# Kernel tuning notes

Measured on AMD Instinct MI355X. Metric: run time of the kernel, lower is better.

Reference implementation:

```python
import jax, jax.numpy as jnp
import numpy as np

STATE_DIM = 64   # state_dim (N), N/2 complex modes
KLEN = 128       # L, learned impulse-response length
CH = 1           # channel_dim
BATCH = 32
T = 1048576      # sequence length (T > L -> FFT branch)
DT_MIN, DT_MAX = 0.001, 0.1


def setup_inputs() -> dict:
    key = jax.random.key(0)
    ks = jax.random.split(key, 7)
    N2 = STATE_DIM // 2
    x = jax.random.normal(ks[0], (BATCH, CH, T), dtype=jnp.float32)
    # HiPPO initialization: w = -0.5 + i * (1/pi) * N * (N/(1+2k) - 1)
    k = np.arange(N2)
    w_real = np.broadcast_to(np.float32(-0.5), (CH, N2)).copy()
    w_imag = np.broadcast_to(
        ((1.0 / np.pi) * STATE_DIM * (STATE_DIM / (1.0 + 2.0 * k) - 1.0)).astype(np.float32),
        (CH, N2)).copy()
    log_dt = (jax.random.uniform(ks[1], (CH, 1), dtype=jnp.float32)
              * (np.log(DT_MAX) - np.log(DT_MIN)) + np.log(DT_MIN))
    C_real = jax.random.normal(ks[2], (CH, 1, N2), dtype=jnp.float32) * 0.1
    C_imag = jax.random.normal(ks[3], (CH, 1, N2), dtype=jnp.float32) * 0.1
    B_real = jax.random.normal(ks[4], (CH, N2), dtype=jnp.float32)
    B_imag = jax.random.normal(ks[5], (CH, N2), dtype=jnp.float32)
    nrm = jnp.sqrt(jnp.sum(B_real ** 2 + B_imag ** 2, axis=-1, keepdims=True))
    B_real, B_imag = B_real / nrm, B_imag / nrm
    D = jax.random.normal(ks[6], (CH,), dtype=jnp.float32) * 0.1
    return {"azimuth_data": x,
            "w_real": jnp.asarray(w_real), "w_imag": jnp.asarray(w_imag),
            "log_dt": log_dt,
            "C_real": C_real, "C_imag": C_imag,
            "B_real": B_real, "B_imag": B_imag,
            "D": D}


def _ssm_kernel(w_real, w_imag, log_dt, C_real, C_imag, B_real, B_imag, D, L):
    """Vectorized equivalent of the per-step power recurrence: h_k = Re(sum_n C_n B_n A_n^k)."""
    w = w_real + 1j * w_imag                      # (CH, N2) complex eigenvalues
    dt = jnp.exp(log_dt)                          # (CH, 1)
    Cc = C_real + 1j * C_imag                     # (CH, 1, N2)
    Bc = B_real + 1j * B_imag                     # (CH, N2)
    dtA = dt[..., None] * w                       # (CH,1,1)*(CH,N2) -> (CH,1,N2)
    # coefficients C.squeeze(1) * B, with the same broadcast as torch: (CH,N2)*(CH,1,N2)->(CH,1,N2)
    coef = jnp.squeeze(Cc, axis=1) * (jnp.ones_like(dtA) * Bc)   # (CH,1,N2)
    ks = jnp.arange(L, dtype=dtA.real.dtype)                      # (L,)
    Ak = jnp.exp(dtA[..., None] * ks)                             # (CH,1,N2,L) = A_discrete**k
    h = jnp.real(jnp.sum(coef[..., None] * Ak, axis=-2))          # (CH,1,L)
    h = h.at[..., 0].add(D)                                       # hk[0] += D (broadcast (CH,1)+(CH,))
    return h[:, None]                                             # unsqueeze(1) -> (CH,1,1,L)


def reference(azimuth_data, w_real, w_imag, log_dt, C_real, C_imag, B_real, B_imag, D):
    Bsz, Cn, Tn = azimuth_data.shape
    kernel = _ssm_kernel(w_real, w_imag, log_dt, C_real, C_imag, B_real, B_imag, D, KLEN)
    pad = KLEN - 1
    x_padded = jnp.pad(azimuth_data, ((0, 0), (0, 0), (pad, 0)))   # causal left-pad
    L_conv = x_padded.shape[-1]
    x_f = jnp.fft.rfft(x_padded, n=L_conv)                         # (B, CH, F)
    k_f = jnp.fft.rfft(kernel, n=L_conv)                           # (CH, 1, 1, F)
    y_f = x_f * k_f                                                # broadcast -> (CH, B, 1, F)
    focused = jnp.fft.irfft(y_f, n=L_conv)[..., :Tn]               # (CH, B, 1, T) — matches torch broadcast
    return focused
```

## Files before the change

### kernel.cpp

```cpp
#include <hip/hip_runtime.h>

#define T_LEN  1048576
#define NROWS  32
#define NTAPS  128
#define N2     32
#define BLOCK  256
#define SEG    4096
#define SEGS_PER_ROW 256
#define HALO   256
#define NCH    11
#define STG_F32 (SEG + HALO)
#define STG_Q4  (STG_F32 / 4)
#define EPI_F32 (32 * 36)

typedef __attribute__((ext_vector_type(8)))  _Float16 half8;
typedef __attribute__((ext_vector_type(2)))  __fp16   fp16x2;
typedef __attribute__((ext_vector_type(16))) float    f32x16;

__device__ __forceinline__ int swz16(int q) { return q ^ ((q >> 3) & 7); }

__global__ __launch_bounds__(NTAPS) void ssm_taps(
    const float* __restrict__ w_real, const float* __restrict__ w_imag,
    const float* __restrict__ log_dt,
    const float* __restrict__ C_real, const float* __restrict__ C_imag,
    const float* __restrict__ B_real, const float* __restrict__ B_imag,
    const float* __restrict__ Dp, float* __restrict__ ws) {
  __shared__ float hsh[NTAPS];
  const int k = threadIdx.x;
  const float dt = expf(log_dt[0]);
  const float kf = (float)k;
  float acc = 0.f;
  for (int n = 0; n < N2; ++n) {
    const float a  = dt * w_real[n];
    const float b  = dt * w_imag[n];
    const float cr = C_real[n], ci = C_imag[n];
    const float br = B_real[n], bi = B_imag[n];
    const float coef_r = cr * br - ci * bi;
    const float coef_i = cr * bi + ci * br;
    const float e = expf(a * kf);
    float s, c;
    sincosf(b * kf, &s, &c);
    acc += e * (coef_r * c - coef_i * s);
  }
  if (k == 0) acc += Dp[0];
  ws[k]  = acc;
  hsh[k] = acc;
  __syncthreads();
  if (k < 64) {
    _Float16* AH = (_Float16*)(ws + NTAPS);
    const int m = k & 31, g = k >> 5;
    for (int c = 0; c < NCH; ++c)
      for (int i = 0; i < 8; ++i) {
        const int idx = m + 129 - 16 * c - 8 * g - i;
        const float v = (idx >= 0 && idx < NTAPS) ? hsh[idx] : 0.f;
        AH[(c * 64 + k) * 8 + i] = (_Float16)v;
      }
  }
}

__global__ __launch_bounds__(BLOCK, 5) void ssm_conv(
    const float* __restrict__ x, const float* __restrict__ ws,
    float* __restrict__ out) {
  __shared__ __align__(16) unsigned char smem[4 * EPI_F32 * 4];

  const int tid  = threadIdx.x;
  const int lane = tid & 63;
  const int wid  = tid >> 6;
  const int p    = lane & 31, g = lane >> 5;
  const int row  = blockIdx.x >> 8;
  const int jb   = blockIdx.x & 255;
  const int n0   = jb * SEG;
  const float* __restrict__ xrow = x + (size_t)row * T_LEN;

  half8 A[NCH];
  const half8* __restrict__ wsA = (const half8*)(ws + NTAPS);
#pragma unroll
  for (int c = 0; c < NCH; ++c) A[c] = wsA[c * 64 + lane];

  _Float16* xh = (_Float16*)smem;
#pragma unroll
  for (int j = 0; j < 5; ++j) {
    const int q4 = tid + 256 * j;
    if (q4 < STG_Q4) {
      int gfi = n0 - HALO + 4 * q4;
      gfi = gfi < 0 ? 0 : gfi;
      const float4 f = *(const float4*)(xrow + gfi);
      const fp16x2 a = __builtin_amdgcn_cvt_pkrtz(f.x, f.y);
      const fp16x2 b = __builtin_amdgcn_cvt_pkrtz(f.z, f.w);
      uint2 w;
      w.x = __builtin_bit_cast(unsigned, a);
      w.y = __builtin_bit_cast(unsigned, b);
      const int c16 = q4 >> 1;
      *(uint2*)((char*)xh + swz16(c16) * 16 + (q4 & 1) * 8) = w;
    }
  }
  __syncthreads();

  const int qb = wid * 128 + 4 * p + g;
  f32x16 acc = {};
#pragma unroll
  for (int c = 0; c < NCH; ++c) {
    const half8 B = *(const half8*)((char*)xh + swz16(qb + 2 * c) * 16);
    acc = __builtin_amdgcn_mfma_f32_32x32x16_f16(A[c], B, acc, 0, 0, 0);
  }
  __syncthreads();

  float* ebuf = (float*)smem + wid * EPI_F32;
#pragma unroll
  for (int k = 0; k < 4; ++k) {
    float4 v;
    v.x = acc[4 * k];     v.y = acc[4 * k + 1];
    v.z = acc[4 * k + 2]; v.w = acc[4 * k + 3];
    *(float4*)(ebuf + p * 36 + 8 * k + 4 * g) = v;
  }
  float* __restrict__ obase = out + (size_t)row * T_LEN + n0 + wid * 1024;
#pragma unroll
  for (int pp = 0; pp < 4; ++pp) {
    const int o  = 4 * lane + 256 * pp;
    const int m0 = o & 31, pc = o >> 5;
    const float4 v = *(const float4*)(ebuf + pc * 36 + m0);
    *(float4*)(obase + o) = v;
  }

  if (jb == 0) {
    __syncthreads();
    const float* __restrict__ h = ws;
    if (tid < 254) {
      float a = 0.f;
      if (tid < 127) {
        for (int k = tid + 1; k < NTAPS; ++k)
          a += h[k] * xrow[T_LEN + tid - k];
      } else {
        for (int k = 0; k <= tid - 127; ++k)
          a += h[k] * xrow[tid - 127 - k];
      }
      out[(size_t)row * T_LEN + tid] = a;
    }
  }
}

extern "C" void kernel_launch(void* const* d_in, const int* in_sizes, int n_in,
                              void* d_out, int out_size, void* d_ws, size_t ws_size,
                              hipStream_t stream) {
  const float* x      = (const float*)d_in[0];
  const float* w_real = (const float*)d_in[1];
  const float* w_imag = (const float*)d_in[2];
  const float* log_dt = (const float*)d_in[3];
  const float* C_real = (const float*)d_in[4];
  const float* C_imag = (const float*)d_in[5];
  const float* B_real = (const float*)d_in[6];
  const float* B_imag = (const float*)d_in[7];
  const float* Dp     = (const float*)d_in[8];
  float* out = (float*)d_out;
  float* ws  = (float*)d_ws;

  ssm_taps<<<1, NTAPS, 0, stream>>>(w_real, w_imag, log_dt,
                                    C_real, C_imag, B_real, B_imag, Dp, ws);
  ssm_conv<<<NROWS * SEGS_PER_ROW, BLOCK, 0, stream>>>(x, ws, out);
}
```

Baseline: 65.75 us.

## Process eight segments per block with double-buffered register prefetch of input

Each block now handles eight consecutive 4096-sample segments instead of one, cutting the grid from 8192 to 1024 blocks. The next segment's global loads go into registers while the current one is computed, and results are converted into a second LDS buffer. This amortizes the per-block tap loads and halo reads and overlaps memory latency with MFMA work. In exchange it raises LDS and register use, lowering occupancy to 4 blocks per SIMD target, and leaves fewer blocks to balance across CUs.

Result: slower. 70.17 us (+6.7%).

```diff
diff --git a/kernel.cpp b/kernel.cpp
--- a/kernel.cpp
+++ b/kernel.cpp
@@ -6,12 +6,13 @@
 #define N2     32
 #define BLOCK  256
 #define SEG    4096
-#define SEGS_PER_ROW 256
+#define SPB    8
 #define HALO   256
 #define NCH    11
 #define STG_F32 (SEG + HALO)
 #define STG_Q4  (STG_F32 / 4)
 #define EPI_F32 (32 * 36)
+#define XH_BYTES 8704
 
 typedef __attribute__((ext_vector_type(8)))  _Float16 half8;
 typedef __attribute__((ext_vector_type(2)))  __fp16   fp16x2;
@@ -58,18 +59,20 @@
   }
 }
 
-__global__ __launch_bounds__(BLOCK, 5) void ssm_conv(
+__global__ __launch_bounds__(BLOCK, 4) void ssm_conv(
     const float* __restrict__ x, const float* __restrict__ ws,
     float* __restrict__ out) {
-  __shared__ __align__(16) unsigned char smem[4 * EPI_F32 * 4];
+  __shared__ __align__(16) unsigned char smem[2 * XH_BYTES + 4 * EPI_F32 * 4];
+  _Float16* xh[2] = {(_Float16*)smem, (_Float16*)(smem + XH_BYTES)};
+  float* ebase = (float*)(smem + 2 * XH_BYTES);
 
   const int tid  = threadIdx.x;
   const int lane = tid & 63;
   const int wid  = tid >> 6;
   const int p    = lane & 31, g = lane >> 5;
-  const int row  = blockIdx.x >> 8;
-  const int jb   = blockIdx.x & 255;
-  const int n0   = jb * SEG;
+  const int row  = blockIdx.x >> 5;
+  const int jb   = blockIdx.x & 31;
+  const int bb   = jb * (SPB * SEG);
   const float* __restrict__ xrow = x + (size_t)row * T_LEN;
 
   half8 A[NCH];
@@ -77,49 +80,73 @@
 #pragma unroll
   for (int c = 0; c < NCH; ++c) A[c] = wsA[c * 64 + lane];
 
-  _Float16* xh = (_Float16*)smem;
+  float4 pf[5];
+  auto loadseg = [&](int sn0) {
 #pragma unroll
-  for (int j = 0; j < 5; ++j) {
-    const int q4 = tid + 256 * j;
-    if (q4 < STG_Q4) {
-      int gfi = n0 - HALO + 4 * q4;
-      gfi = gfi < 0 ? 0 : gfi;
-      const float4 f = *(const float4*)(xrow + gfi);
-      const fp16x2 a = __builtin_amdgcn_cvt_pkrtz(f.x, f.y);
-      const fp16x2 b = __builtin_amdgcn_cvt_pkrtz(f.z, f.w);
-      uint2 w;
-      w.x = __builtin_bit_cast(unsigned, a);
-      w.y = __builtin_bit_cast(unsigned, b);
-      const int c16 = q4 >> 1;
-      *(uint2*)((char*)xh + swz16(c16) * 16 + (q4 & 1) * 8) = w;
+    for (int j = 0; j < 5; ++j) {
+      const int q4 = tid + 256 * j;
+      if (q4 < STG_Q4) {
+        int gfi = sn0 - HALO + 4 * q4;
+        gfi = gfi < 0 ? 0 : gfi;
+        pf[j] = *(const float4*)(xrow + gfi);
+      }
     }
-  }
+  };
+  auto cvtwrite = [&](_Float16* dst) {
+#pragma unroll
+    for (int j = 0; j < 5; ++j) {
+      const int q4 = tid + 256 * j;
+      if (q4 < STG_Q4) {
+        const fp16x2 a = __builtin_amdgcn_cvt_pkrtz(pf[j].x, pf[j].y);
+        const fp16x2 b = __builtin_amdgcn_cvt_pkrtz(pf[j].z, pf[j].w);
+        uint2 w;
+        w.x = __builtin_bit_cast(unsigned, a);
+        w.y = __builtin_bit_cast(unsigned, b);
+        const int c16 = q4 >> 1;
+        *(uint2*)((char*)dst + swz16(c16) * 16 + (q4 & 1) * 8) = w;
+      }
+    }
+  };
+
+  loadseg(bb);
+  cvtwrite(xh[0]);
+  loadseg(bb + SEG);
   __syncthreads();
 
   const int qb = wid * 128 + 4 * p + g;
-  f32x16 acc = {};
 #pragma unroll
-  for (int c = 0; c < NCH; ++c) {
-    const half8 B = *(const half8*)((char*)xh + swz16(qb + 2 * c) * 16);
-    acc = __builtin_amdgcn_mfma_f32_32x32x16_f16(A[c], B, acc, 0, 0, 0);
-  }
-  __syncthreads();
+  for (int s = 0; s < SPB; ++s) {
+    const _Float16* xr = xh[s & 1];
 
-  float* ebuf = (float*)smem + wid * EPI_F32;
+    f32x16 acc = {};
 #pragma unroll
-  for (int k = 0; k < 4; ++k) {
-    float4 v;
-    v.x = acc[4 * k];     v.y = acc[4 * k + 1];
-    v.z = acc[4 * k + 2]; v.w = acc[4 * k + 3];
-    *(float4*)(ebuf + p * 36 + 8 * k + 4 * g) = v;
-  }
-  float* __restrict__ obase = out + (size_t)row * T_LEN + n0 + wid * 1024;
+    for (int c = 0; c < NCH; ++c) {
+      const half8 B = *(const half8*)((const char*)xr + swz16(qb + 2 * c) * 16);
+      acc = __builtin_amdgcn_mfma_f32_32x32x16_f16(A[c], B, acc, 0, 0, 0);
+    }
+
+    float* ebuf = ebase + wid * EPI_F32;
 #pragma unroll
-  for (int pp = 0; pp < 4; ++pp) {
-    const int o  = 4 * lane + 256 * pp;
-    const int m0 = o & 31, pc = o >> 5;
-    const float4 v = *(const float4*)(ebuf + pc * 36 + m0);
-    *(float4*)(obase + o) = v;
+    for (int k = 0; k < 4; ++k) {
+      float4 v;
+      v.x = acc[4 * k];     v.y = acc[4 * k + 1];
+      v.z = acc[4 * k + 2]; v.w = acc[4 * k + 3];
+      *(float4*)(ebuf + p * 36 + 8 * k + 4 * g) = v;
+    }
+    float* __restrict__ obase = out + (size_t)row * T_LEN + bb + s * SEG + wid * 1024;
+#pragma unroll
+    for (int pp = 0; pp < 4; ++pp) {
+      const int o  = 4 * lane + 256 * pp;
+      const int m0 = o & 31, pc = o >> 5;
+      const float4 v = *(const float4*)(ebuf + pc * 36 + m0);
+      *(float4*)(obase + o) = v;
+    }
+
+    if (s + 1 < SPB) {
+      cvtwrite(xh[(s + 1) & 1]);
+      if (s + 2 < SPB) loadseg(bb + (s + 2) * SEG);
+      __syncthreads();
+    }
   }
 
   if (jb == 0) {
@@ -156,5 +183,5 @@
 
   ssm_taps<<<1, NTAPS, 0, stream>>>(w_real, w_imag, log_dt,
                                     C_real, C_imag, B_real, B_imag, Dp, ws);
-  ssm_conv<<<NROWS * SEGS_PER_ROW, BLOCK, 0, stream>>>(x, ws, out);
+  ssm_conv<<<NROWS * 32, BLOCK, 0, stream>>>(x, ws, out);
 }
```
